# Performance work log

Measured on AMD Instinct MI355X. Metric: run time of the kernel, lower is better.

The kernel has to match this reference:

```python
import jax, jax.numpy as jnp
import numpy as np

B, T, F, H = 4096, 8, 64, 64          # batch(=edges), time windows, feat_dim, attention hidden
N, De = 2048, 128                      # graph nodes, node/edge feature dim
NF, NC = 64, 2                         # conv filters, num classes
HID1, HID2 = 256, 24                   # LazyLinear dims
FLAT = NF * T * 2 * F                  # flattened conv output


def setup_inputs() -> dict:
    key = jax.random.key(0)
    ks = jax.random.split(key, 25)
    rn = lambda k, shape, s=0.05: jax.random.normal(k, shape, jnp.float32) * s
    return {
        "X_nume": jax.random.normal(ks[0], (B, T, F), jnp.float32),
        "src": jax.random.randint(ks[1], (B,), 0, N, jnp.int32),
        "dst": jax.random.randint(ks[2], (B,), 0, N, jnp.int32),
        "node_feat": jax.random.normal(ks[3], (N, De), jnp.float32),
        "edge_feat": jax.random.normal(ks[4], (B, De), jnp.float32),
        # attention params (original uses uniform(0,1); scaled uniform here)
        "attn_W": jax.random.uniform(ks[5], (F, H), jnp.float32) * 0.1,
        "attn_U": jax.random.uniform(ks[6], (F, H), jnp.float32) * 0.1,
        "attn_V": jax.random.uniform(ks[7], (H, 1), jnp.float32) * 0.1,
        # conv
        "conv_w": rn(ks[8], (NF, 1, 2, 2)), "conv_b": rn(ks[9], (NF,)),
        # GraphConv 1/2 (weights stored [in, out])
        "gc1_W": rn(ks[10], (De, 128)), "gc1_b": rn(ks[11], (128,)),
        "gc2_W": rn(ks[12], (128, 8)), "gc2_b": rn(ks[13], (8,)),
        # edge linears
        "lin1_W": rn(ks[14], (De, 128)), "lin1_b": rn(ks[15], (128,)),
        "lin2_W": rn(ks[16], (128, 8)), "lin2_b": rn(ks[17], (8,)),
        # MLP head
        "fc1_W": rn(ks[18], (FLAT, HID1), 0.01), "fc1_b": rn(ks[19], (HID1,)),
        "fc2_W": rn(ks[20], (HID1, HID2)), "fc2_b": rn(ks[21], (HID2,)),
        "fc3_W": rn(ks[22], (HID2 + 24, NC)), "fc3_b": rn(ks[23], (NC,)),
    }


def _graph_conv(h, W, b, src, dst, n):
    # DGL GraphConv, norm='both': out = D_in^{-1/2} A D_out^{-1/2} h W + b
    ones = jnp.ones(src.shape[0], h.dtype)
    deg_out = jnp.clip(jax.ops.segment_sum(ones, src, num_segments=n), 1.0)
    deg_in = jnp.clip(jax.ops.segment_sum(ones, dst, num_segments=n), 1.0)
    hs = h * jax.lax.rsqrt(deg_out)[:, None]
    agg = jax.ops.segment_sum(hs[src], dst, num_segments=n)  # [N, in]
    agg = agg * jax.lax.rsqrt(deg_in)[:, None]
    return agg @ W + b


def _forward(X_nume, src, dst, node_feat, edge_feat,
             attn_W, attn_U, attn_V, conv_w, conv_b,
             gc1_W, gc1_b, gc2_W, gc2_b, lin1_W, lin1_b, lin2_W, lin2_b,
             fc1_W, fc1_b, fc2_W, fc2_b, fc3_W, fc3_b):
    # ---- temporal attention (vectorized O(T^2)) ----
    a = jnp.einsum('btf,fh->bth', X_nume, attn_W)   # x_i W
    u = jnp.einsum('btf,fh->bth', X_nume, attn_U)   # x_j U
    # e[b,i,j] = tanh(a_i + u_j) @ V  -> [B,T,T]
    e = jnp.einsum('bijh,h->bij', jnp.tanh(a[:, :, None, :] + u[:, None, :, :]), attn_V[:, 0])
    alpha = jax.nn.softmax(e, axis=2)
    # c_i = sum_{j != i} alpha_ij x_j  (softmax over all j, self term excluded from sum)
    ctx = jnp.einsum('bij,bjf->bif', alpha, X_nume)
    diag = jnp.diagonal(alpha, axis1=1, axis2=2)    # [B,T]
    ctx = ctx - diag[:, :, None] * X_nume
    att_out = jnp.concatenate([X_nume, ctx], axis=-1)  # [B,T,2F]

    # ---- CNN ----
    conv_in = att_out[:, None, :, :]  # [B,1,T,2F]
    conv_out = jax.lax.conv_general_dilated(
        conv_in, conv_w, window_strides=(1, 1), padding='SAME',
        dimension_numbers=('NCHW', 'OIHW', 'NCHW')) + conv_b[None, :, None, None]
    conv_out = jax.nn.relu(conv_out)  # [B,NF,T,2F]

    # ---- dual GraphConv message passing ----
    h1 = jax.nn.relu(_graph_conv(node_feat, gc1_W, gc1_b, src, dst, N))
    e1 = jax.nn.relu(edge_feat @ lin1_W + lin1_b)
    h2 = _graph_conv(h1, gc2_W, gc2_b, src, dst, N)   # no relu (matches source)
    e2 = jax.nn.relu(e1 @ lin2_W + lin2_b)
    edge_x = h2[src] + h2[dst] + e2                    # [E,8]
    node_feats = jnp.stack([h2[src], h2[dst], edge_x], axis=1).reshape(B, -1)  # [B,24]

    # ---- MLP head ----
    out = conv_out.reshape(B, -1)
    out = jax.nn.relu(out @ fc1_W + fc1_b)
    out = jax.nn.relu(out @ fc2_W + fc2_b)
    out = jnp.concatenate([out, node_feats], axis=1)
    return out @ fc3_W + fc3_b  # [B, NC]


def reference(X_nume, src, dst, node_feat, edge_feat,
              attn_W, attn_U, attn_V, conv_w, conv_b,
              gc1_W, gc1_b, gc2_W, gc2_b, lin1_W, lin1_b, lin2_W, lin2_b,
              fc1_W, fc1_b, fc2_W, fc2_b, fc3_W, fc3_b):
    return _forward(X_nume, src, dst, node_feat, edge_feat,
                    attn_W, attn_U, attn_V, conv_w, conv_b,
                    gc1_W, gc1_b, gc2_W, gc2_b, lin1_W, lin1_b, lin2_W, lin2_b,
                    fc1_W, fc1_b, fc2_W, fc2_b, fc3_W, fc3_b)
```

## Files before the change

### kernel.cpp

```cpp
#include <hip/hip_runtime.h>
#include <stdint.h>
#include <stddef.h>

typedef float    f32x4  __attribute__((ext_vector_type(4)));
typedef short    bf16x8 __attribute__((ext_vector_type(8)));
typedef uint16_t u16x8  __attribute__((ext_vector_type(8)));
typedef uint32_t u32x4  __attribute__((ext_vector_type(4)));

#define ATT_ROW 136

__device__ __forceinline__ uint16_t f2bf(float x) {
  union { float f; uint32_t u; } c; c.f = x;
  return (uint16_t)((c.u + 0x7FFFu + ((c.u >> 16) & 1u)) >> 16);
}
__device__ __forceinline__ float bf2f(uint16_t h) {
  union { uint32_t u; float f; } c; c.u = ((uint32_t)h) << 16;
  return c.f;
}
__device__ __forceinline__ int S64s(int a) { return a ^ (((a >> 6) & 7) << 4); }

__device__ __forceinline__ void cp16(void* lds, const void* g) {
  __builtin_amdgcn_global_load_lds((const __attribute__((address_space(1))) void*)g,
                                   (__attribute__((address_space(3))) void*)lds, 16, 0, 0);
}
__device__ __forceinline__ float fast_tanh(float t) {
  float r = __expf(-2.f * t);
  return 1.f - 2.f * r / (1.f + r);
}

__global__ __launch_bounds__(256) void k_prep(const float* __restrict__ W1,
                                              uint16_t* __restrict__ W1s) {
  __shared__ float st[32 * 256];
  const int c = blockIdx.x, tid = threadIdx.x;
  const float* src = W1 + (size_t)c * 32 * 256;
#pragma unroll
  for (int it = 0; it < 8; ++it) {
    int u = it * 256 + tid;
    ((f32x4*)st)[u] = ((const f32x4*)src)[u];
  }
  __syncthreads();
  uint16_t* dstc = W1s + (size_t)c * 8192;
#pragma unroll
  for (int q = 0; q < 4; ++q) {
    int p  = q * 256 + tid;
    int Np = p >> 2, Gp = p & 3;
    int n  = Np ^ ((Np >> 2) & 1);
    int g  = Gp ^ (n & 3);
    uint32_t w[4];
#pragma unroll
    for (int e2 = 0; e2 < 4; ++e2) {
      uint16_t lo = f2bf(st[(g * 8 + 2 * e2) * 256 + n]);
      uint16_t hi = f2bf(st[(g * 8 + 2 * e2 + 1) * 256 + n]);
      w[e2] = (uint32_t)lo | ((uint32_t)hi << 16);
    }
    u32x4 v; v.x = w[0]; v.y = w[1]; v.z = w[2]; v.w = w[3];
    *(u32x4*)(dstc + (size_t)p * 8) = v;
  }
}

__global__ __launch_bounds__(512) void k_att(const float* __restrict__ X,
    const float* __restrict__ aW, const float* __restrict__ aU,
    const float* __restrict__ aV, uint16_t* __restrict__ att) {
  __shared__ float sa[8][8][66];
  __shared__ float su[8][8][66];
  __shared__ float sal[8][64];
  __shared__ float sv[64];
  const int tid = threadIdx.x, lane = tid & 63, w = tid >> 6;
  if (tid < 64) sv[tid] = aV[tid];
  __syncthreads();
  for (int rep = 0; rep < 2; ++rep) {
    int b  = blockIdx.x * 16 + w * 2 + rep;
    int bu = __builtin_amdgcn_readfirstlane(b);
    const float* xb = X + (size_t)bu * 512;
    float xi[8];
#pragma unroll
    for (int i = 0; i < 8; ++i) xi[i] = xb[i * 64 + lane];
    float a[8], u[8];
#pragma unroll
    for (int i = 0; i < 8; ++i) { a[i] = 0.f; u[i] = 0.f; }
#pragma unroll
    for (int f = 0; f < 64; ++f) {
      float wf = aW[f * 64 + lane];
      float uf = aU[f * 64 + lane];
#pragma unroll
      for (int i = 0; i < 8; ++i) {
        float xs = xb[i * 64 + f];
        a[i] = fmaf(xs, wf, a[i]);
        u[i] = fmaf(xs, uf, u[i]);
      }
    }
#pragma unroll
    for (int i = 0; i < 8; ++i) { sa[w][i][lane] = a[i]; su[w][i][lane] = u[i]; }
    __syncthreads();
    int i2 = lane >> 3, j2 = lane & 7;
    float ev = 0.f;
#pragma unroll
    for (int h = 0; h < 64; ++h)
      ev = fmaf(fast_tanh(sa[w][i2][h] + su[w][j2][h]), sv[h], ev);
    float m = ev;
    m = fmaxf(m, __shfl_xor(m, 1));
    m = fmaxf(m, __shfl_xor(m, 2));
    m = fmaxf(m, __shfl_xor(m, 4));
    float p = __expf(ev - m);
    float s = p;
    s += __shfl_xor(s, 1); s += __shfl_xor(s, 2); s += __shfl_xor(s, 4);
    sal[w][lane] = p / s;
    __syncthreads();
#pragma unroll
    for (int i = 0; i < 8; ++i) {
      float c = 0.f;
#pragma unroll
      for (int j = 0; j < 8; ++j) c = fmaf(sal[w][i * 8 + j], xi[j], c);
      c = fmaf(-sal[w][i * 8 + i], xi[i], c);
      size_t ro = ((size_t)b * 9 + i) * ATT_ROW;
      att[ro + lane]      = f2bf(xi[i]);
      att[ro + 64 + lane] = f2bf(c);
      if (lane < 8) att[ro + 128 + lane] = 0;
    }
    {
      size_t ro = ((size_t)b * 9 + 8) * ATT_ROW;
      att[ro + lane] = 0; att[ro + 64 + lane] = 0;
      if (lane < 8) att[ro + 128 + lane] = 0;
    }
    __syncthreads();
  }
}

__global__ void k_deg(const int* __restrict__ src, const int* __restrict__ dst,
                      float* degO, float* degI) {
  int t = blockIdx.x * 256 + threadIdx.x;
  if (t < 4096) {
    atomicAdd(degO + src[t], 1.f);
    atomicAdd(degI + dst[t], 1.f);
  }
}
__global__ __launch_bounds__(256) void k_gca(const float* __restrict__ h,
    const int* __restrict__ src, const int* __restrict__ dst,
    const float* __restrict__ degO, float* __restrict__ agg) {
  int t = blockIdx.x * 256 + threadIdx.x;
  int e = t >> 7, d = t & 127;
  int s = src[e];
  float sc = rsqrtf(fmaxf(degO[s], 1.f));
  atomicAdd(agg + (size_t)dst[e] * 128 + d, h[(size_t)s * 128 + d] * sc);
}
__global__ __launch_bounds__(128) void k_gc1b(const float* __restrict__ agg,
    const float* __restrict__ degI, const float* __restrict__ Wt,
    const float* __restrict__ bs, float* __restrict__ h1) {
  __shared__ float vs[128];
  int n = blockIdx.x, t = threadIdx.x;
  float sc = rsqrtf(fmaxf(degI[n], 1.f));
  vs[t] = agg[(size_t)n * 128 + t] * sc;
  __syncthreads();
  float acc = bs[t];
#pragma unroll 8
  for (int d = 0; d < 128; ++d) acc = fmaf(vs[d], Wt[d * 128 + t], acc);
  h1[(size_t)n * 128 + t] = fmaxf(acc, 0.f);
}
__global__ __launch_bounds__(128) void k_gc2b(const float* __restrict__ agg,
    const float* __restrict__ degI, const float* __restrict__ Wt,
    const float* __restrict__ bs, float* __restrict__ h2) {
  __shared__ float vs[128];
  int n = blockIdx.x, t = threadIdx.x;
  float sc = rsqrtf(fmaxf(degI[n], 1.f));
  vs[t] = agg[(size_t)n * 128 + t] * sc;
  __syncthreads();
  if (t < 8) {
    float acc = bs[t];
#pragma unroll 8
    for (int d = 0; d < 128; ++d) acc = fmaf(vs[d], Wt[d * 8 + t], acc);
    h2[(size_t)n * 8 + t] = acc;
  }
}
__global__ __launch_bounds__(128) void k_e12(const float* __restrict__ ef,
    const float* __restrict__ W1, const float* __restrict__ b1,
    const float* __restrict__ W2, const float* __restrict__ b2,
    float* __restrict__ e2) {
  __shared__ float efs[128];
  __shared__ float t1s[128];
  int t = threadIdx.x;
  for (int it = 0; it < 16; ++it) {
    int b = blockIdx.x * 16 + it;
    efs[t] = ef[(size_t)b * 128 + t];
    __syncthreads();
    float acc = b1[t];
#pragma unroll 8
    for (int d = 0; d < 128; ++d) acc = fmaf(efs[d], W1[d * 128 + t], acc);
    t1s[t] = fmaxf(acc, 0.f);
    __syncthreads();
    if (t < 8) {
      float a2 = b2[t];
#pragma unroll 8
      for (int h = 0; h < 128; ++h) a2 = fmaf(t1s[h], W2[h * 8 + t], a2);
      e2[(size_t)b * 8 + t] = fmaxf(a2, 0.f);
    }
    __syncthreads();
  }
}

#define NS 64
struct Win { u16x8 a0, b0; uint16_t ae, be; };

__global__ __launch_bounds__(512, 4) void k_gemm(const uint16_t* __restrict__ W1s,
    const uint16_t* __restrict__ att, const float* __restrict__ conv_w,
    const float* __restrict__ conv_b, float* __restrict__ out1) {
  __shared__ __align__(16) char smem[65536];
  char* Abuf = smem;
  char* Bbuf = smem + 16384;

  const int tid = threadIdx.x;
  const int lane = tid & 63, ln15 = lane & 15, g = lane >> 4;
  const int wid = tid >> 6, wm = wid >> 2, wn = wid & 3;
  const int bid = blockIdx.x;
  const int i_row = bid & 7, oh = (bid >> 3) & 1, jh = (bid >> 4) & 1;
  const int btile = bid >> 5;
  const int b0 = btile * 128;
  const int am = tid >> 2, ag = tid & 3;

  f32x4 acc[4][4];
#pragma unroll
  for (int mt = 0; mt < 4; ++mt)
#pragma unroll
    for (int nt = 0; nt < 4; ++nt) { f32x4 z = {0.f, 0.f, 0.f, 0.f}; acc[mt][nt] = z; }

  auto loadWin = [&](int ss) {
    int jg = jh * 2 + (ss & 1);
    int j0 = jg * 32 + ag * 8;
    const uint16_t* r0 = att + ((size_t)(b0 + am) * 9 + i_row) * ATT_ROW + j0;
    const uint16_t* r1 = r0 + ATT_ROW;
    Win w;
    w.a0 = *(const u16x8*)r0; w.ae = r0[8];
    w.b0 = *(const u16x8*)r1; w.be = r1[8];
    return w;
  };

  auto computeA = [&](const Win& w, int ss, char* Ab) {
    float t0[9], t1[9];
#pragma unroll
    for (int e = 0; e < 8; ++e) {
      t0[e] = bf2f((uint16_t)w.a0[e]);
      t1[e] = bf2f((uint16_t)w.b0[e]);
    }
    t0[8] = bf2f(w.ae); t1[8] = bf2f(w.be);
    int o = oh * 32 + (ss >> 1);
    float c0  = conv_b[o];
    float k00 = conv_w[o * 4 + 0], k01 = conv_w[o * 4 + 1];
    float k10 = conv_w[o * 4 + 2], k11 = conv_w[o * 4 + 3];
    uint32_t pk[4];
#pragma unroll
    for (int e2 = 0; e2 < 8; e2 += 2) {
      float v0 = fmaf(k00, t0[e2],     fmaf(k01, t0[e2 + 1], fmaf(k10, t1[e2],     fmaf(k11, t1[e2 + 1], c0))));
      float v1 = fmaf(k00, t0[e2 + 1], fmaf(k01, t0[e2 + 2], fmaf(k10, t1[e2 + 1], fmaf(k11, t1[e2 + 2], c0))));
      v0 = fmaxf(v0, 0.f); v1 = fmaxf(v1, 0.f);
      uint32_t pr;
      asm("v_cvt_pk_bf16_f32 %0, %1, %2" : "=v"(pr) : "v"(v0), "v"(v1));
      pk[e2 >> 1] = pr;
    }
    u32x4 wv; wv.x = pk[0]; wv.y = pk[1]; wv.z = pk[2]; wv.w = pk[3];
    *(u32x4*)(Ab + S64s(am * 64 + ag * 16)) = wv;
  };

  auto stageB = [&](int ss, char* Bb) {
    int jg = jh * 2 + (ss & 1);
    int c = (oh * 32 + (ss >> 1)) * 32 + i_row * 4 + jg;
    const char* gsrc = (const char*)W1s + (size_t)c * 16384;
#pragma unroll
    for (int it = 0; it < 2; ++it) {
      char* ldsb = Bb + (size_t)(it * 512 + (tid & ~63)) * 16;
      cp16(ldsb, gsrc + (size_t)(it * 512 + tid) * 16);
    }
  };

  auto mfmaStep = [&](const char* Ab, const char* Bb) {
    bf16x8 bfr[4];
#pragma unroll
    for (int nt = 0; nt < 4; ++nt) {
      int n = wn * 64 + nt * 16 + ln15;
      bfr[nt] = *(const bf16x8*)(Bb + S64s(n * 64 + g * 16));
    }
    bf16x8 afr[4];
#pragma unroll
    for (int mt = 0; mt < 4; ++mt) {
      int m = wm * 64 + mt * 16 + ln15;
      afr[mt] = *(const bf16x8*)(Ab + S64s(m * 64 + g * 16));
    }
#pragma unroll
    for (int mt = 0; mt < 4; ++mt)
#pragma unroll
      for (int nt = 0; nt < 4; ++nt)
        acc[mt][nt] = __builtin_amdgcn_mfma_f32_16x16x32_bf16(afr[mt], bfr[nt], acc[mt][nt], 0, 0, 0);
  };

  stageB(0, Bbuf);
  stageB(1, Bbuf + 16384);
  Win w0 = loadWin(0);
  computeA(w0, 0, Abuf);
  Win wc = loadWin(1);
  asm volatile("s_waitcnt lgkmcnt(0)" ::: "memory");
  __builtin_amdgcn_sched_barrier(0);
  __builtin_amdgcn_s_barrier();
  __builtin_amdgcn_sched_barrier(0);

#pragma unroll 1
  for (int ss = 0; ss < NS; ++ss) {
    if (ss + 2 < NS) stageB(ss + 2, Bbuf + ((ss + 2) % 3) * 16384);
    Win wn = wc;
    if (ss + 2 < NS) wn = loadWin(ss + 2);
    if (ss + 1 < NS) computeA(wc, ss + 1, Abuf + ((ss + 1) & 1) * 8192);
    wc = wn;
    mfmaStep(Abuf + (ss & 1) * 8192, Bbuf + (ss % 3) * 16384);
    asm volatile("s_waitcnt vmcnt(6)" ::: "memory");
    asm volatile("s_waitcnt lgkmcnt(0)" ::: "memory");
    __builtin_amdgcn_sched_barrier(0);
    __builtin_amdgcn_s_barrier();
    __builtin_amdgcn_sched_barrier(0);
  }

  const int rbase = b0 + wm * 64 + (lane >> 4) * 4;
  const int cbase = wn * 64 + ln15;
#pragma unroll
  for (int mt = 0; mt < 4; ++mt)
#pragma unroll
    for (int nt = 0; nt < 4; ++nt)
#pragma unroll
      for (int r = 0; r < 4; ++r)
        atomicAdd(out1 + (size_t)(rbase + mt * 16 + r) * 256 + cbase + nt * 16,
                  acc[mt][nt][r]);
}

__global__ __launch_bounds__(512) void k_fin(const float* __restrict__ out1,
    const float* __restrict__ fc1_b, const float* __restrict__ fc2_W,
    const float* __restrict__ fc2_b, const float* __restrict__ fc3_W,
    const float* __restrict__ fc3_b, const int* __restrict__ src,
    const int* __restrict__ dst, const float* __restrict__ h2,
    const float* __restrict__ e2, float* __restrict__ outp) {
  int lane = threadIdx.x & 63, w = threadIdx.x >> 6;
  int b  = blockIdx.x * 8 + w;
  int bu = __builtin_amdgcn_readfirstlane(b);
  f32x4 o4 = ((const f32x4*)(out1 + (size_t)bu * 256))[lane];
  f32x4 bi = ((const f32x4*)fc1_b)[lane];
  float v[4];
#pragma unroll
  for (int r = 0; r < 4; ++r) v[r] = fmaxf(o4[r] + bi[r], 0.f);
  float a24[24];
#pragma unroll
  for (int q = 0; q < 24; ++q) a24[q] = 0.f;
#pragma unroll
  for (int r = 0; r < 4; ++r) {
    const float* wr = fc2_W + (size_t)(lane * 4 + r) * 24;
#pragma unroll
    for (int q = 0; q < 24; ++q) a24[q] = fmaf(v[r], wr[q], a24[q]);
  }
#pragma unroll
  for (int q = 0; q < 24; ++q) {
    float t = a24[q];
    t += __shfl_xor(t, 1);  t += __shfl_xor(t, 2);  t += __shfl_xor(t, 4);
    t += __shfl_xor(t, 8);  t += __shfl_xor(t, 16); t += __shfl_xor(t, 32);
    a24[q] = fmaxf(t + fc2_b[q], 0.f);
  }
  int s = src[bu], d2 = dst[bu];
  float nf[24];
#pragma unroll
  for (int q = 0; q < 8; ++q) {
    float hs = h2[(size_t)s * 8 + q];
    float hd = h2[(size_t)d2 * 8 + q];
    nf[q] = hs; nf[8 + q] = hd; nf[16 + q] = hs + hd + e2[(size_t)bu * 8 + q];
  }
  if (lane == 0) {
#pragma unroll
    for (int c = 0; c < 2; ++c) {
      float r = fc3_b[c];
#pragma unroll
      for (int q = 0; q < 24; ++q) r = fmaf(a24[q], fc3_W[q * 2 + c], r);
#pragma unroll
      for (int q = 0; q < 24; ++q) r = fmaf(nf[q], fc3_W[(24 + q) * 2 + c], r);
      outp[(size_t)bu * 2 + c] = r;
    }
  }
}

extern "C" void kernel_launch(void* const* d_in, const int* in_sizes, int n_in,
                              void* d_out, int out_size, void* d_ws, size_t ws_size,
                              hipStream_t stream) {
  const float* X         = (const float*)d_in[0];
  const int*   src       = (const int*)d_in[1];
  const int*   dst       = (const int*)d_in[2];
  const float* node_feat = (const float*)d_in[3];
  const float* edge_feat = (const float*)d_in[4];
  const float* attn_W    = (const float*)d_in[5];
  const float* attn_U    = (const float*)d_in[6];
  const float* attn_V    = (const float*)d_in[7];
  const float* conv_w    = (const float*)d_in[8];
  const float* conv_b    = (const float*)d_in[9];
  const float* gc1_W     = (const float*)d_in[10];
  const float* gc1_b     = (const float*)d_in[11];
  const float* gc2_W     = (const float*)d_in[12];
  const float* gc2_b     = (const float*)d_in[13];
  const float* lin1_W    = (const float*)d_in[14];
  const float* lin1_b    = (const float*)d_in[15];
  const float* lin2_W    = (const float*)d_in[16];
  const float* lin2_b    = (const float*)d_in[17];
  const float* fc1_W     = (const float*)d_in[18];
  const float* fc1_b     = (const float*)d_in[19];
  const float* fc2_W     = (const float*)d_in[20];
  const float* fc2_b     = (const float*)d_in[21];
  const float* fc3_W     = (const float*)d_in[22];
  const float* fc3_b     = (const float*)d_in[23];

  char* ws = (char*)d_ws;
  float*    out1 = (float*)(ws + 0);
  float*    agg1 = (float*)(ws + 4194304);
  float*    agg2 = (float*)(ws + 5242880);
  float*    degO = (float*)(ws + 6291456);
  float*    degI = (float*)(ws + 6299648);
  uint16_t* W1s  = (uint16_t*)(ws + 6307840);
  uint16_t* att  = (uint16_t*)(ws + 39862272);
  float*    h1   = (float*)(ws + 49889280);
  float*    h2   = (float*)(ws + 50937856);
  float*    e2   = (float*)(ws + 51003392);

  hipMemsetAsync(d_ws, 0, 6307840, stream);

  k_prep<<<dim3(2048), dim3(256), 0, stream>>>(fc1_W, W1s);
  k_att <<<dim3(256),  dim3(512), 0, stream>>>(X, attn_W, attn_U, attn_V, att);
  k_deg <<<dim3(16),   dim3(256), 0, stream>>>(src, dst, degO, degI);
  k_gca <<<dim3(2048), dim3(256), 0, stream>>>(node_feat, src, dst, degO, agg1);
  k_gc1b<<<dim3(2048), dim3(128), 0, stream>>>(agg1, degI, gc1_W, gc1_b, h1);
  k_gca <<<dim3(2048), dim3(256), 0, stream>>>(h1, src, dst, degO, agg2);
  k_gc2b<<<dim3(2048), dim3(128), 0, stream>>>(agg2, degI, gc2_W, gc2_b, h2);
  k_e12 <<<dim3(256),  dim3(128), 0, stream>>>(edge_feat, lin1_W, lin1_b, lin2_W, lin2_b, e2);
  k_gemm<<<dim3(1024), dim3(512), 0, stream>>>(W1s, att, conv_w, conv_b, out1);
  k_fin <<<dim3(512),  dim3(512), 0, stream>>>(out1, fc1_b, fc2_W, fc2_b, fc3_W, fc3_b,
                                               src, dst, h2, e2, (float*)d_out);
}
```

Baseline: 554.1 us.

## Load fc1 weight fragments directly to registers and double K per step

The fc1 GEMM kernel stops staging weight tiles through LDS with async global-to-LDS copies. Each wave now reads its B fragments straight from global memory into registers, double-buffered across steps. Each block handles both column halves (jh merged), so every step covers a K of 64 instead of 32. This halves the grid to 512 blocks and cuts the number of barriers and the atomic output traffic. The cost is more registers per thread, since the occupancy hint is dropped and 16 B vectors are live, plus uncoalesced direct global fragment loads that rely on the cache.

```diff
diff --git a/kernel.cpp b/kernel.cpp
--- a/kernel.cpp
+++ b/kernel.cpp
@@ -19,10 +19,6 @@
 }
 __device__ __forceinline__ int S64s(int a) { return a ^ (((a >> 6) & 7) << 4); }
 
-__device__ __forceinline__ void cp16(void* lds, const void* g) {
-  __builtin_amdgcn_global_load_lds((const __attribute__((address_space(1))) void*)g,
-                                   (__attribute__((address_space(3))) void*)lds, 16, 0, 0);
-}
 __device__ __forceinline__ float fast_tanh(float t) {
   float r = __expf(-2.f * t);
   return 1.f - 2.f * r / (1.f + r);
@@ -197,57 +193,61 @@
   }
 }
 
-#define NS 64
-struct Win { u16x8 a0, b0; uint16_t ae, be; };
-
-__global__ __launch_bounds__(512, 4) void k_gemm(const uint16_t* __restrict__ W1s,
+__global__ __launch_bounds__(512) void k_gemm(const uint16_t* __restrict__ W1s,
     const uint16_t* __restrict__ att, const float* __restrict__ conv_w,
     const float* __restrict__ conv_b, float* __restrict__ out1) {
-  __shared__ __align__(16) char smem[65536];
-  char* Abuf = smem;
-  char* Bbuf = smem + 16384;
+  __shared__ __align__(16) char smem[32768];
 
   const int tid = threadIdx.x;
   const int lane = tid & 63, ln15 = lane & 15, g = lane >> 4;
-  const int wid = tid >> 6, wm = wid >> 2, wn = wid & 3;
+  const int wid = tid >> 6, wm = wid >> 2, wvn = wid & 3;
   const int bid = blockIdx.x;
-  const int i_row = bid & 7, oh = (bid >> 3) & 1, jh = (bid >> 4) & 1;
-  const int btile = bid >> 5;
+  const int i_row = bid & 7, oh = (bid >> 3) & 1;
+  const int btile = bid >> 4;
   const int b0 = btile * 128;
   const int am = tid >> 2, ag = tid & 3;
 
+  const uint16_t* rb = att + ((size_t)(b0 + am) * 9 + i_row) * ATT_ROW + ag * 16;
+  const char* W1c = (const char*)W1s + ((size_t)(oh * 32) * 32 + i_row * 4) * 16384;
+  int voff[4], aro[4];
+#pragma unroll
+  for (int nt = 0; nt < 4; ++nt)
+    voff[nt] = S64s((wvn * 64 + nt * 16 + ln15) * 64 + g * 16);
+#pragma unroll
+  for (int mt = 0; mt < 4; ++mt)
+    aro[mt] = S64s((wm * 64 + mt * 16 + ln15) * 64 + g * 16);
+  const int aw0 = (ag >> 1) * 8192 + S64s(am * 64 + (ag & 1) * 32);
+
   f32x4 acc[4][4];
 #pragma unroll
   for (int mt = 0; mt < 4; ++mt)
 #pragma unroll
     for (int nt = 0; nt < 4; ++nt) { f32x4 z = {0.f, 0.f, 0.f, 0.f}; acc[mt][nt] = z; }
 
-  auto loadWin = [&](int ss) {
-    int jg = jh * 2 + (ss & 1);
-    int j0 = jg * 32 + ag * 8;
-    const uint16_t* r0 = att + ((size_t)(b0 + am) * 9 + i_row) * ATT_ROW + j0;
+  struct Win { u16x8 a0, a1, b0, b1; uint16_t ae, be; };
+  auto loadWin = [&](int h) {
+    const uint16_t* r0 = rb + h * 64;
     const uint16_t* r1 = r0 + ATT_ROW;
     Win w;
-    w.a0 = *(const u16x8*)r0; w.ae = r0[8];
-    w.b0 = *(const u16x8*)r1; w.be = r1[8];
+    w.a0 = *(const u16x8*)r0; w.a1 = *(const u16x8*)(r0 + 8); w.ae = r0[16];
+    w.b0 = *(const u16x8*)r1; w.b1 = *(const u16x8*)(r1 + 8); w.be = r1[16];
     return w;
   };
 
-  auto computeA = [&](const Win& w, int ss, char* Ab) {
-    float t0[9], t1[9];
+  auto computeA = [&](const Win& w, int o, char* As) {
+    float t0[17], t1[17];
 #pragma unroll
     for (int e = 0; e < 8; ++e) {
-      t0[e] = bf2f((uint16_t)w.a0[e]);
-      t1[e] = bf2f((uint16_t)w.b0[e]);
-    }
-    t0[8] = bf2f(w.ae); t1[8] = bf2f(w.be);
-    int o = oh * 32 + (ss >> 1);
+      t0[e] = bf2f((uint16_t)w.a0[e]); t0[e + 8] = bf2f((uint16_t)w.a1[e]);
+      t1[e] = bf2f((uint16_t)w.b0[e]); t1[e + 8] = bf2f((uint16_t)w.b1[e]);
+    }
+    t0[16] = bf2f(w.ae); t1[16] = bf2f(w.be);
     float c0  = conv_b[o];
     float k00 = conv_w[o * 4 + 0], k01 = conv_w[o * 4 + 1];
     float k10 = conv_w[o * 4 + 2], k11 = conv_w[o * 4 + 3];
-    uint32_t pk[4];
-#pragma unroll
-    for (int e2 = 0; e2 < 8; e2 += 2) {
+    uint32_t pk[8];
+#pragma unroll
+    for (int e2 = 0; e2 < 16; e2 += 2) {
       float v0 = fmaf(k00, t0[e2],     fmaf(k01, t0[e2 + 1], fmaf(k10, t1[e2],     fmaf(k11, t1[e2 + 1], c0))));
       float v1 = fmaf(k00, t0[e2 + 1], fmaf(k01, t0[e2 + 2], fmaf(k10, t1[e2 + 1], fmaf(k11, t1[e2 + 2], c0))));
       v0 = fmaxf(v0, 0.f); v1 = fmaxf(v1, 0.f);
@@ -255,68 +255,89 @@
       asm("v_cvt_pk_bf16_f32 %0, %1, %2" : "=v"(pr) : "v"(v0), "v"(v1));
       pk[e2 >> 1] = pr;
     }
-    u32x4 wv; wv.x = pk[0]; wv.y = pk[1]; wv.z = pk[2]; wv.w = pk[3];
-    *(u32x4*)(Ab + S64s(am * 64 + ag * 16)) = wv;
+    u32x4 wv0; wv0.x = pk[0]; wv0.y = pk[1]; wv0.z = pk[2]; wv0.w = pk[3];
+    u32x4 wv1; wv1.x = pk[4]; wv1.y = pk[5]; wv1.z = pk[6]; wv1.w = pk[7];
+    *(u32x4*)(As + aw0)        = wv0;
+    *(u32x4*)(As + (aw0 ^ 16)) = wv1;
   };
 
-  auto stageB = [&](int ss, char* Bb) {
-    int jg = jh * 2 + (ss & 1);
-    int c = (oh * 32 + (ss >> 1)) * 32 + i_row * 4 + jg;
-    const char* gsrc = (const char*)W1s + (size_t)c * 16384;
-#pragma unroll
-    for (int it = 0; it < 2; ++it) {
-      char* ldsb = Bb + (size_t)(it * 512 + (tid & ~63)) * 16;
-      cp16(ldsb, gsrc + (size_t)(it * 512 + tid) * 16);
+  auto mfmaStep = [&](const char* As, const bf16x8* bank) {
+#pragma unroll
+    for (int kk = 0; kk < 2; ++kk) {
+      bf16x8 afr[4];
+#pragma unroll
+      for (int mt = 0; mt < 4; ++mt)
+        afr[mt] = *(const bf16x8*)(As + kk * 8192 + aro[mt]);
+#pragma unroll
+      for (int mt = 0; mt < 4; ++mt)
+#pragma unroll
+        for (int nt = 0; nt < 4; ++nt)
+          acc[mt][nt] = __builtin_amdgcn_mfma_f32_16x16x32_bf16(afr[mt], bank[kk * 4 + nt], acc[mt][nt], 0, 0, 0);
     }
   };
 
-  auto mfmaStep = [&](const char* Ab, const char* Bb) {
-    bf16x8 bfr[4];
-#pragma unroll
-    for (int nt = 0; nt < 4; ++nt) {
-      int n = wn * 64 + nt * 16 + ln15;
-      bfr[nt] = *(const bf16x8*)(Bb + S64s(n * 64 + g * 16));
-    }
-    bf16x8 afr[4];
-#pragma unroll
-    for (int mt = 0; mt < 4; ++mt) {
-      int m = wm * 64 + mt * 16 + ln15;
-      afr[mt] = *(const bf16x8*)(Ab + S64s(m * 64 + g * 16));
-    }
-#pragma unroll
-    for (int mt = 0; mt < 4; ++mt)
-#pragma unroll
-      for (int nt = 0; nt < 4; ++nt)
-        acc[mt][nt] = __builtin_amdgcn_mfma_f32_16x16x32_bf16(afr[mt], bfr[nt], acc[mt][nt], 0, 0, 0);
-  };
-
-  stageB(0, Bbuf);
-  stageB(1, Bbuf + 16384);
-  Win w0 = loadWin(0);
-  computeA(w0, 0, Abuf);
-  Win wc = loadWin(1);
+  bf16x8 bA[8], bB[8];
+  Win winC, winN;
+
+#pragma unroll
+  for (int nt = 0; nt < 4; ++nt) {
+    bA[nt]     = *(const bf16x8*)(W1c + voff[nt]);
+    bA[4 + nt] = *(const bf16x8*)(W1c + 16384 + voff[nt]);
+  }
+  {
+    Win w0 = loadWin(0);
+    computeA(w0, oh * 32, smem);
+  }
+  winC = loadWin(1);
+  winN = winC;
   asm volatile("s_waitcnt lgkmcnt(0)" ::: "memory");
   __builtin_amdgcn_sched_barrier(0);
   __builtin_amdgcn_s_barrier();
   __builtin_amdgcn_sched_barrier(0);
 
+#define GEMM_STEP(CUR, NXT, CB1, H2, O1, ARD, AWR, DO_L)                         \
+  {                                                                              \
+    _Pragma("unroll") for (int nt = 0; nt < 4; ++nt) {                           \
+      NXT[nt]     = *(const bf16x8*)((CB1) + voff[nt]);                          \
+      NXT[4 + nt] = *(const bf16x8*)((CB1) + 16384 + voff[nt]);                  \
+    }                                                                            \
+    if (DO_L) winN = loadWin(H2);                                                \
+    computeA(winC, (O1), (AWR));                                                 \
+    winC = winN;                                                                 \
+    mfmaStep((ARD), CUR);                                                        \
+    asm volatile("s_waitcnt lgkmcnt(0)" ::: "memory");                           \
+    __builtin_amdgcn_sched_barrier(0);                                           \
+    __builtin_amdgcn_s_barrier();                                                \
+    __builtin_amdgcn_sched_barrier(0);                                           \
+  }
+
+  const char* cb = W1c;
+  int oc = oh * 32;
 #pragma unroll 1
-  for (int ss = 0; ss < NS; ++ss) {
-    if (ss + 2 < NS) stageB(ss + 2, Bbuf + ((ss + 2) % 3) * 16384);
-    Win wn = wc;
-    if (ss + 2 < NS) wn = loadWin(ss + 2);
-    if (ss + 1 < NS) computeA(wc, ss + 1, Abuf + ((ss + 1) & 1) * 8192);
-    wc = wn;
-    mfmaStep(Abuf + (ss & 1) * 8192, Bbuf + (ss % 3) * 16384);
-    asm volatile("s_waitcnt vmcnt(6)" ::: "memory");
+  for (int it = 0; it < 31; ++it) {
+    GEMM_STEP(bA, bB, cb + 32768, 0, oc, smem, smem + 16384, 1)
+    GEMM_STEP(bB, bA, cb + 524288, 1, oc + 1, smem + 16384, smem, 1)
+    cb += 524288;
+    ++oc;
+  }
+  {
+#pragma unroll
+    for (int nt = 0; nt < 4; ++nt) {
+      bB[nt]     = *(const bf16x8*)(cb + 32768 + voff[nt]);
+      bB[4 + nt] = *(const bf16x8*)(cb + 32768 + 16384 + voff[nt]);
+    }
+    computeA(winC, oh * 32 + 31, smem + 16384);
+    mfmaStep(smem, bA);
     asm volatile("s_waitcnt lgkmcnt(0)" ::: "memory");
     __builtin_amdgcn_sched_barrier(0);
     __builtin_amdgcn_s_barrier();
     __builtin_amdgcn_sched_barrier(0);
   }
+  mfmaStep(smem + 16384, bB);
+#undef GEMM_STEP
 
   const int rbase = b0 + wm * 64 + (lane >> 4) * 4;
-  const int cbase = wn * 64 + ln15;
+  const int cbase = wvn * 64 + ln15;
 #pragma unroll
   for (int mt = 0; mt < 4; ++mt)
 #pragma unroll
@@ -428,7 +449,7 @@
   k_gca <<<dim3(2048), dim3(256), 0, stream>>>(h1, src, dst, degO, agg2);
   k_gc2b<<<dim3(2048), dim3(128), 0, stream>>>(agg2, degI, gc2_W, gc2_b, h2);
   k_e12 <<<dim3(256),  dim3(128), 0, stream>>>(edge_feat, lin1_W, lin1_b, lin2_W, lin2_b, e2);
-  k_gemm<<<dim3(1024), dim3(512), 0, stream>>>(W1s, att, conv_w, conv_b, out1);
+  k_gemm<<<dim3(512),  dim3(512), 0, stream>>>(W1s, att, conv_w, conv_b, out1);
   k_fin <<<dim3(512),  dim3(512), 0, stream>>>(out1, fc1_b, fc2_W, fc2_b, fc3_W, fc3_b,
                                                src, dst, h2, e2, (float*)d_out);
 }
```

Measured after the change: 520.4 us. -6.1%, faster.
